# Kernel tuning notes

Measured on AMD Instinct MI355X. Metric: run time of the kernel, lower is better.

Reference implementation:

```python
import jax, jax.numpy as jnp
import numpy as np

N_NODES = 100000
N_EDGES = 1600000
IN_FEATS = 16
H_FEAT = 64
N_HEADS = 3
N_LAYERS = 8
NUM_CLASSES = 6
HID = H_FEAT * N_HEADS  # 192
NEG_SLOPE = 0.01  # torch F.leaky_relu default


def setup_inputs() -> dict:
    key = jax.random.key(0)
    ks = jax.random.split(key, 10)
    node_feat = jax.random.normal(ks[0], (N_NODES, IN_FEATS), dtype=jnp.float32)
    src = jax.random.randint(ks[1], (N_EDGES,), 0, N_NODES)
    dst = jax.random.randint(ks[2], (N_EDGES,), 0, N_NODES)
    # layer 1 params: per-head fc [H, out, in], attn [H, 2*out]
    W1 = jax.random.normal(ks[3], (N_HEADS, H_FEAT, IN_FEATS), dtype=jnp.float32) * 0.1
    a1 = jax.random.normal(ks[4], (N_HEADS, 2 * H_FEAT), dtype=jnp.float32) * 0.1
    # layers 2..8 params stacked: [L-1, H, out, hid]
    W = jax.random.normal(ks[5], (N_LAYERS - 1, N_HEADS, H_FEAT, HID), dtype=jnp.float32) * 0.1
    a = jax.random.normal(ks[6], (N_LAYERS - 1, N_HEADS, 2 * H_FEAT), dtype=jnp.float32) * 0.1
    fcW = jax.random.normal(ks[7], (NUM_CLASSES, HID), dtype=jnp.float32) * 0.1
    fcb = jnp.zeros((NUM_CLASSES,), dtype=jnp.float32)
    return {"node_feat": node_feat, "src": src, "dst": dst,
            "W1": W1, "a1": a1, "W": W, "a": a, "fcW": fcW, "fcb": fcb}


def _gat_layer(h, src, dst, Wl, al, n_nodes):
    """Multi-head GAT layer (merge='cat'). Wl:[H,O,I], al:[H,2O]."""
    O = Wl.shape[1]
    z = jnp.einsum('ni,hoi->nho', h, Wl)            # [N,H,O]
    a_src, a_dst = al[:, :O], al[:, O:]
    # attn_fc(cat(z_src, z_dst)) decomposed into per-node src/dst scores
    es = jnp.einsum('nho,ho->nh', z, a_src)          # [N,H]
    ed = jnp.einsum('nho,ho->nh', z, a_dst)          # [N,H]
    e = jax.nn.leaky_relu(es[src] + ed[dst], NEG_SLOPE)  # [E,H]
    # segment softmax over incoming edges of each dst node
    m = jax.ops.segment_max(e, dst, num_segments=n_nodes)
    m = jnp.where(jnp.isfinite(m), m, 0.0)
    ex = jnp.exp(e - m[dst])
    den = jax.ops.segment_sum(ex, dst, num_segments=n_nodes)
    alpha = ex / jnp.maximum(den[dst], 1e-9)          # [E,H]
    # scatter-sum aggregation of alpha-weighted source features
    hn = jax.ops.segment_sum(alpha[:, :, None] * z[src], dst, num_segments=n_nodes)  # [N,H,O]
    return hn.reshape(n_nodes, -1)                    # cat heads -> [N,H*O]


def reference(node_feat, src, dst, W1, a1, W, a, fcW, fcb):
    n = node_feat.shape[0]
    h = _gat_layer(node_feat, src, dst, W1, a1, n)
    h = jax.nn.elu(h)
    for l in range(W.shape[0]):
        h = _gat_layer(h, src, dst, W[l], a[l], n)
        h = jax.nn.elu(h)
    return h @ fcW.T + fcb
```

## Files before the change

### kernel.cpp

```cpp
#include <hip/hip_runtime.h>
#include <hip/hip_bf16.h>
#include <hip/hip_fp16.h>
#include <math.h>

#define NN 100000
#define NE 1600000
#define INF_ 16
#define HF 64
#define NH 3
#define HID 192
#define NC 6
#define NEG_SLOPE 0.01f

typedef _Float16 half8 __attribute__((ext_vector_type(8)));
typedef float f32x4 __attribute__((ext_vector_type(4)));


__global__ __launch_bounds__(256) void k_hist(const int* __restrict__ dst, int* __restrict__ deg) {
    int e = blockIdx.x * 256 + threadIdx.x;
    if (e < NE) atomicAdd(&deg[dst[e]], 1);
}

__global__ __launch_bounds__(256) void k_scan1(const int* __restrict__ deg, int* __restrict__ bsum) {
    __shared__ int sc[256];
    int t = threadIdx.x;
    int n = blockIdx.x * 256 + t;
    int v = (n < NN) ? deg[n] : 0;
    sc[t] = v; __syncthreads();
    for (int off = 1; off < 256; off <<= 1) {
        int x = (t >= off) ? sc[t - off] : 0;
        __syncthreads();
        sc[t] += x;
        __syncthreads();
    }
    if (t == 255) bsum[blockIdx.x] = sc[255];
}

__global__ __launch_bounds__(512) void k_scan2(const int* __restrict__ bsum, int* __restrict__ boff, int nb) {
    __shared__ int sc[512];
    int t = threadIdx.x;
    int v = (t < nb) ? bsum[t] : 0;
    sc[t] = v; __syncthreads();
    for (int off = 1; off < 512; off <<= 1) {
        int x = (t >= off) ? sc[t - off] : 0;
        __syncthreads();
        sc[t] += x;
        __syncthreads();
    }
    if (t < nb) boff[t] = sc[t] - v;
}

__global__ __launch_bounds__(256) void k_scan3(const int* __restrict__ deg, const int* __restrict__ boff,
                                               int* __restrict__ row_ptr, int* __restrict__ cursor) {
    __shared__ int sc[256];
    int t = threadIdx.x;
    int n = blockIdx.x * 256 + t;
    int v = (n < NN) ? deg[n] : 0;
    sc[t] = v; __syncthreads();
    for (int off = 1; off < 256; off <<= 1) {
        int x = (t >= off) ? sc[t - off] : 0;
        __syncthreads();
        sc[t] += x;
        __syncthreads();
    }
    if (n < NN) {
        int ex = boff[blockIdx.x] + sc[t] - v;
        row_ptr[n] = ex;
        cursor[n] = ex;
        if (n == NN - 1) row_ptr[NN] = ex + v;
    }
}

__global__ __launch_bounds__(256) void k_scatter(const int* __restrict__ src, const int* __restrict__ dst,
                                                 int* __restrict__ cursor, int* __restrict__ colb) {
    int e = blockIdx.x * 256 + threadIdx.x;
    if (e < NE) {
        int d = dst[e];
        int pos = atomicAdd(&cursor[d], 1);
        colb[pos] = src[e] * 384;
    }
}


__global__ __launch_bounds__(256) void k_cvtW(const float* __restrict__ W, __half* __restrict__ Wh, int n) {
    int i = blockIdx.x * 256 + threadIdx.x;
    if (i < n) Wh[i] = __float2half(W[i]);
}


__global__ __launch_bounds__(256) void k_prep(const float* __restrict__ W1, const float* __restrict__ a1,
                                              const float* __restrict__ W, const float* __restrict__ a,
                                              float* __restrict__ v0, __half* __restrict__ vh) {
    int bid = blockIdx.x, tid = threadIdx.x;
    if (bid == 0) {
        if (tid < 96) {
            int j = tid >> 4, k = tid & 15;
            int h = j % 3, sd = j / 3;
            float s = 0.f;
            for (int c = 0; c < 64; ++c)
                s += W1[h * 1024 + c * 16 + k] * a1[h * 128 + sd * 64 + c];
            v0[j * 16 + k] = s;
        }
    } else {
        int l = bid - 1;
        if (tid < HID) {
            int k = tid;
            __half* vt = vh + (size_t)l * 16 * HID;
            for (int j = 0; j < 6; ++j) {
                int h = j % 3, sd = j / 3;
                const float* wp = W + (size_t)l * 36864 + h * 12288 + k;
                const float* ap = a + (size_t)l * 384 + h * 128 + sd * 64;
                float s = 0.f;
                for (int c = 0; c < 64; ++c) s += wp[c * 192] * ap[c];
                __half hi = __float2half(s);
                __half lo = __float2half(s - __half2float(hi));
                vt[j * HID + k] = hi;
                vt[(j + 6) * HID + k] = lo;
            }
            for (int j = 12; j < 16; ++j) vt[j * HID + k] = __float2half(0.f);
        }
    }
}


__global__ __launch_bounds__(256) void k_transform1(const float* __restrict__ feat, const float* __restrict__ W1,
                                                    __half* __restrict__ zh) {
    int idx = blockIdx.x * 256 + threadIdx.x;
    if (idx >= NN * HID) return;
    int n = idx / HID;
    int c = idx - n * HID;
    const float* fr = feat + n * INF_;
    const float* wr = W1 + c * INF_;
    float s = 0.f;
#pragma unroll
    for (int i = 0; i < INF_; i += 4) {
        float4 f = *(const float4*)&fr[i];
        float4 w = *(const float4*)&wr[i];
        s += f.x * w.x + f.y * w.y + f.z * w.z + f.w * w.w;
    }
    zh[idx] = __float2half(s);
}


__global__ __launch_bounds__(256) void k_esed1(const float* __restrict__ feat, const float* __restrict__ v0,
                                               float* __restrict__ es, float* __restrict__ ed) {
    __shared__ float sv[96];
    int tid = threadIdx.x;
    if (tid < 96) sv[tid] = v0[tid];
    __syncthreads();
    int n = blockIdx.x * 256 + tid;
    if (n >= NN) return;
    float f[16];
#pragma unroll
    for (int i = 0; i < 16; i += 4) {
        float4 t4 = *(const float4*)&feat[n * 16 + i];
        f[i] = t4.x; f[i + 1] = t4.y; f[i + 2] = t4.z; f[i + 3] = t4.w;
    }
#pragma unroll
    for (int j = 0; j < 6; ++j) {
        float s = 0.f;
#pragma unroll
        for (int k = 0; k < 16; ++k) s += f[k] * sv[j * 16 + k];
        if (j < 3) es[n * 3 + j] = s;
        else ed[n * 3 + (j - 3)] = s;
    }
}


__global__ __launch_bounds__(256) void k_mfma(const __half* __restrict__ Ah, const __half* __restrict__ Whl,
                                              const __half* __restrict__ vhl,
                                              __half* __restrict__ zh, float* __restrict__ es,
                                              float* __restrict__ ed) {
    __shared__ char Bs[73728];
    int tid = threadIdx.x;

#pragma unroll
    for (int i = 0; i < 18; ++i) {
        int idx = tid + i * 256;
        int row = idx / 24;
        int pos = idx - row * 24;
        uint4 v = *(const uint4*)((const char*)Whl + (size_t)idx * 16);
        *(uint4*)(Bs + row * 384 + ((pos * 16) ^ ((row & 7) << 4))) = v;
    }
    __syncthreads();

    int wid = tid >> 6;
    int lane = tid & 63;
    int lrow = lane & 15;
    int lk = lane >> 4;
    int r0 = blockIdx.x * 128 + wid * 32;

    int arow0 = min(r0 + lrow, NN - 1);
    int arow1 = min(r0 + 16 + lrow, NN - 1);
    const __half* ap0 = &Ah[(size_t)arow0 * HID];
    const __half* ap1 = &Ah[(size_t)arow1 * HID];

    f32x4 acc[2][12];
    f32x4 acc13[2];
#pragma unroll
    for (int f = 0; f < 2; ++f) {
        acc13[f] = (f32x4){0.f, 0.f, 0.f, 0.f};
#pragma unroll
        for (int t = 0; t < 12; ++t) acc[f][t] = (f32x4){0.f, 0.f, 0.f, 0.f};
    }

#pragma unroll
    for (int ks = 0; ks < 6; ++ks) {
        half8 a0 = *(const half8*)&ap0[ks * 32 + lk * 8];
        half8 a1 = *(const half8*)&ap1[ks * 32 + lk * 8];
        half8 b13 = *(const half8*)&vhl[lrow * HID + ks * 32 + lk * 8];
        acc13[0] = __builtin_amdgcn_mfma_f32_16x16x32_f16(a0, b13, acc13[0], 0, 0, 0);
        acc13[1] = __builtin_amdgcn_mfma_f32_16x16x32_f16(a1, b13, acc13[1], 0, 0, 0);
#pragma unroll
        for (int t = 0; t < 12; ++t) {
            int brow = t * 16 + lrow;
            half8 bf = *(const half8*)(Bs + brow * 384 + ((ks * 64 + lk * 16) ^ ((brow & 7) << 4)));
            acc[0][t] = __builtin_amdgcn_mfma_f32_16x16x32_f16(a0, bf, acc[0][t], 0, 0, 0);
            acc[1][t] = __builtin_amdgcn_mfma_f32_16x16x32_f16(a1, bf, acc[1][t], 0, 0, 0);
        }
    }

#pragma unroll
    for (int f = 0; f < 2; ++f) {
        int orow0 = r0 + f * 16 + lk * 4;
#pragma unroll
        for (int t = 0; t < 12; ++t) {
#pragma unroll
            for (int g = 0; g < 4; ++g) {
                int row = orow0 + g;
                if (row < NN) zh[(size_t)row * HID + t * 16 + lrow] = __float2half(acc[f][t][g]);
            }
        }
#pragma unroll
        for (int g = 0; g < 4; ++g) {
            float vhi = acc13[f][g];
            float vlo = __shfl(vhi, lane + 6);
            float tot = vhi + vlo;
            int row = orow0 + g;
            if (row < NN) {
                if (lrow < 3) es[row * NH + lrow] = tot;
                else if (lrow < 6) ed[row * NH + (lrow - 3)] = tot;
            }
        }
    }
}


__global__ __launch_bounds__(256) void k_agg(const __half* __restrict__ zh, const int* __restrict__ colb,
                                             const float* __restrict__ es, const float* __restrict__ ed,
                                             const int* __restrict__ row_ptr, __half* __restrict__ h_out) {
    int w = blockIdx.x * 4 + (threadIdx.x >> 6);
    int slot = (threadIdx.x >> 3) & 7;
    int q = threadIdx.x & 7;
    int n = w * 8 + slot;
    int beg = row_ptr[n];
    int deg = row_ptr[n + 1] - beg;

    float3 d3 = *(const float3*)((const char*)ed + n * 12);

    float l0 = 0.f, l1 = 0.f, l2 = 0.f;
    float a0[8], a1[8], a2[8];
#pragma unroll
    for (int k = 0; k < 8; ++k) { a0[k] = 0.f; a1[k] = 0.f; a2[k] = 0.f; }

    const int* cp = colb + beg;
    const char* zb = (const char*)zh + q * 16;

    int so_n = 0;
    float3 s3_n = make_float3(0.f, 0.f, 0.f);
    if (deg > 0) {
        so_n = cp[0];
        s3_n = *(const float3*)((const char*)es + (so_n >> 5));
    }
    for (int i = 0; i < deg; ++i) {
        int so = so_n;
        float3 s3 = s3_n;
        if (i + 1 < deg) {
            so_n = cp[i + 1];
            s3_n = *(const float3*)((const char*)es + (so_n >> 5));
        }
        float x0 = s3.x + d3.x, x1 = s3.y + d3.y, x2 = s3.z + d3.z;
        x0 = fmaxf(x0, NEG_SLOPE * x0);
        x1 = fmaxf(x1, NEG_SLOPE * x1);
        x2 = fmaxf(x2, NEG_SLOPE * x2);
        float p0 = __expf(x0), p1 = __expf(x1), p2 = __expf(x2);
        const char* zp = zb + so;
        half8 z0 = *(const half8*)(zp);
        half8 z1 = *(const half8*)(zp + 128);
        half8 z2 = *(const half8*)(zp + 256);
        l0 += p0; l1 += p1; l2 += p2;
#pragma unroll
        for (int k = 0; k < 8; ++k) {
            a0[k] += p0 * (float)z0[k];
            a1[k] += p1 * (float)z1[k];
            a2[k] += p2 * (float)z2[k];
        }
    }

    float r0 = 1.f / fmaxf(l0, 1e-9f);
    float r1 = 1.f / fmaxf(l1, 1e-9f);
    float r2 = 1.f / fmaxf(l2, 1e-9f);
    char* ob = (char*)h_out + (size_t)n * 384 + q * 16;
    union { float4 f4; __half2 h2[4]; } u;
#pragma unroll
    for (int k = 0; k < 4; ++k) {
        float x0 = a0[2 * k] * r0, x1 = a0[2 * k + 1] * r0;
        x0 = (x0 > 0.f) ? x0 : (__expf(x0) - 1.f);
        x1 = (x1 > 0.f) ? x1 : (__expf(x1) - 1.f);
        u.h2[k] = __floats2half2_rn(x0, x1);
    }
    *(float4*)ob = u.f4;
#pragma unroll
    for (int k = 0; k < 4; ++k) {
        float x0 = a1[2 * k] * r1, x1 = a1[2 * k + 1] * r1;
        x0 = (x0 > 0.f) ? x0 : (__expf(x0) - 1.f);
        x1 = (x1 > 0.f) ? x1 : (__expf(x1) - 1.f);
        u.h2[k] = __floats2half2_rn(x0, x1);
    }
    *(float4*)(ob + 128) = u.f4;
#pragma unroll
    for (int k = 0; k < 4; ++k) {
        float x0 = a2[2 * k] * r2, x1 = a2[2 * k + 1] * r2;
        x0 = (x0 > 0.f) ? x0 : (__expf(x0) - 1.f);
        x1 = (x1 > 0.f) ? x1 : (__expf(x1) - 1.f);
        u.h2[k] = __floats2half2_rn(x0, x1);
    }
    *(float4*)(ob + 256) = u.f4;
}


__device__ inline float wred_sum(float v) {
#pragma unroll
    for (int o = 32; o; o >>= 1) v += __shfl_xor(v, o);
    return v;
}

__global__ __launch_bounds__(256) void k_fc(const __half* __restrict__ hbuf, const float* __restrict__ fcW,
                                            const float* __restrict__ fcb, float* __restrict__ out) {
    __shared__ float sW[NC * HID];
    __shared__ float sb[NC];
    int tid = threadIdx.x;
    for (int i = tid; i < NC * HID; i += 256) sW[i] = fcW[i];
    if (tid < NC) sb[tid] = fcb[tid];
    __syncthreads();
    int w = tid >> 6;
    int lane = tid & 63;
    int n = blockIdx.x * 4 + w;
    if (n >= NN) return;
    float h0 = __half2float(hbuf[(size_t)n * HID + lane]);
    float h1 = __half2float(hbuf[(size_t)n * HID + 64 + lane]);
    float h2 = __half2float(hbuf[(size_t)n * HID + 128 + lane]);
#pragma unroll
    for (int j = 0; j < NC; ++j) {
        float p = h0 * sW[j * HID + lane] + h1 * sW[j * HID + 64 + lane] + h2 * sW[j * HID + 128 + lane];
        p = wred_sum(p);
        if (lane == 0) out[n * NC + j] = p + sb[j];
    }
}


extern "C" void kernel_launch(void* const* d_in, const int* in_sizes, int n_in,
                              void* d_out, int out_size, void* d_ws, size_t ws_size,
                              hipStream_t stream) {
    const float* node_feat = (const float*)d_in[0];
    const int* src = (const int*)d_in[1];
    const int* dst = (const int*)d_in[2];
    const float* W1 = (const float*)d_in[3];
    const float* a1 = (const float*)d_in[4];
    const float* W = (const float*)d_in[5];
    const float* a = (const float*)d_in[6];
    const float* fcW = (const float*)d_in[7];
    const float* fcb = (const float*)d_in[8];
    float* out = (float*)d_out;

    char* p = (char*)d_ws;
    auto alloc = [&](size_t bytes) {
        void* r = (void*)p;
        p += (bytes + 255) & ~(size_t)255;
        return r;
    };
    int* deg = (int*)alloc(NN * 4);
    int* cursor = (int*)alloc(NN * 4);
    int* row_ptr = (int*)alloc((NN + 1) * 4);
    int* bsum = (int*)alloc(512 * 4);
    int* boff = (int*)alloc(512 * 4);
    int* colb = (int*)alloc((size_t)NE * 4);
    float* es = (float*)alloc((size_t)NN * NH * 4);
    float* ed = (float*)alloc((size_t)NN * NH * 4);
    __half* zh = (__half*)alloc((size_t)NN * HID * 2);
    __half* hb = (__half*)alloc((size_t)NN * HID * 2);
    const int NWH = 7 * NH * HF * HID;
    __half* Wh = (__half*)alloc((size_t)NWH * 2);
    float* v0 = (float*)alloc(96 * 4);
    __half* vh = (__half*)alloc((size_t)7 * 16 * HID * 2);

    int nb = (NN + 255) / 256;

    hipMemsetAsync(deg, 0, NN * 4, stream);
    k_hist<<<(NE + 255) / 256, 256, 0, stream>>>(dst, deg);
    k_scan1<<<nb, 256, 0, stream>>>(deg, bsum);
    k_scan2<<<1, 512, 0, stream>>>(bsum, boff, nb);
    k_scan3<<<nb, 256, 0, stream>>>(deg, boff, row_ptr, cursor);
    k_scatter<<<(NE + 255) / 256, 256, 0, stream>>>(src, dst, cursor, colb);
    k_cvtW<<<(NWH + 255) / 256, 256, 0, stream>>>(W, Wh, NWH);
    k_prep<<<8, 256, 0, stream>>>(W1, a1, W, a, v0, vh);

    int gAgg = NN / 8 / 4;

    k_transform1<<<(NN * HID + 255) / 256, 256, 0, stream>>>(node_feat, W1, zh);
    k_esed1<<<nb, 256, 0, stream>>>(node_feat, v0, es, ed);
    k_agg<<<gAgg, 256, 0, stream>>>(zh, colb, es, ed, row_ptr, hb);

    for (int l = 0; l < 7; ++l) {
        k_mfma<<<(NN + 127) / 128, 256, 0, stream>>>(hb, Wh + (size_t)l * NH * HF * HID,
                                                     vh + (size_t)l * 16 * HID, zh, es, ed);
        k_agg<<<gAgg, 256, 0, stream>>>(zh, colb, es, ed, row_ptr, hb);
    }

    k_fc<<<(NN + 3) / 4, 256, 0, stream>>>(hb, fcW, fcb, out);
}
```

Baseline: 1.395 ms.

## Build CSR via two-pass bucketed scatter and unroll aggregation by two edges

Replaces the per-edge global atomic scatter into CSR with a two-pass scheme. Edges are first binned by destination into 512-node buckets using shared-memory counters and staged as packed (local dst, src) words. A per-bucket kernel then places them using shared-memory cursors, which localizes the atomics and the writes. Separately, the aggregation loop processes two edges per iteration so more gathers are in flight, at the cost of more registers and an extra staging buffer.

Result: faster. 1.307 ms (-6.3%).

```diff
diff --git a/kernel.cpp b/kernel.cpp
--- a/kernel.cpp
+++ b/kernel.cpp
@@ -12,6 +12,10 @@
 #define NC 6
 #define NEG_SLOPE 0.01f
 
+#define BSH 9
+#define NBUCK 196
+#define TILE 2048
+
 typedef _Float16 half8 __attribute__((ext_vector_type(8)));
 typedef float f32x4 __attribute__((ext_vector_type(4)));
 
@@ -51,7 +55,7 @@
 }
 
 __global__ __launch_bounds__(256) void k_scan3(const int* __restrict__ deg, const int* __restrict__ boff,
-                                               int* __restrict__ row_ptr, int* __restrict__ cursor) {
+                                               int* __restrict__ row_ptr) {
     __shared__ int sc[256];
     int t = threadIdx.x;
     int n = blockIdx.x * 256 + t;
@@ -66,18 +70,67 @@
     if (n < NN) {
         int ex = boff[blockIdx.x] + sc[t] - v;
         row_ptr[n] = ex;
-        cursor[n] = ex;
         if (n == NN - 1) row_ptr[NN] = ex + v;
     }
 }
 
-__global__ __launch_bounds__(256) void k_scatter(const int* __restrict__ src, const int* __restrict__ dst,
-                                                 int* __restrict__ cursor, int* __restrict__ colb) {
-    int e = blockIdx.x * 256 + threadIdx.x;
-    if (e < NE) {
-        int d = dst[e];
-        int pos = atomicAdd(&cursor[d], 1);
-        colb[pos] = src[e] * 384;
+__global__ __launch_bounds__(256) void k_binit(const int* __restrict__ row_ptr, int* __restrict__ gcur) {
+    int b = threadIdx.x;
+    if (b < NBUCK) gcur[b] = row_ptr[min(b << BSH, NN)];
+}
+
+__global__ __launch_bounds__(256) void k_bucket(const int* __restrict__ src, const int* __restrict__ dst,
+                                                int* __restrict__ gcur, int* __restrict__ staged) {
+    __shared__ int cnt[NBUCK], base[NBUCK], cnt2[NBUCK];
+    int tid = threadIdx.x;
+    int e0 = blockIdx.x * TILE;
+    int cntE = min(TILE, NE - e0);
+    for (int i = tid; i < NBUCK; i += 256) { cnt[i] = 0; cnt2[i] = 0; }
+    __syncthreads();
+    int myDst[8], mySrc[8];
+#pragma unroll
+    for (int k = 0; k < 8; ++k) {
+        int idx = tid + k * 256;
+        if (idx < cntE) {
+            myDst[k] = dst[e0 + idx];
+            mySrc[k] = src[e0 + idx];
+            atomicAdd(&cnt[myDst[k] >> BSH], 1);
+        }
+    }
+    __syncthreads();
+    for (int i = tid; i < NBUCK; i += 256) {
+        if (cnt[i] > 0) base[i] = atomicAdd(&gcur[i], cnt[i]);
+    }
+    __syncthreads();
+#pragma unroll
+    for (int k = 0; k < 8; ++k) {
+        int idx = tid + k * 256;
+        if (idx < cntE) {
+            int b = myDst[k] >> BSH;
+            int r = atomicAdd(&cnt2[b], 1);
+            staged[base[b] + r] = ((myDst[k] & 511) << 17) | mySrc[k];
+        }
+    }
+}
+
+__global__ __launch_bounds__(256) void k_bscatter(const int* __restrict__ row_ptr, const int* __restrict__ staged,
+                                                  int* __restrict__ colb) {
+    __shared__ int cur[512];
+    int b = blockIdx.x;
+    int n0 = b << BSH;
+    int tid = threadIdx.x;
+    for (int i = tid; i < 512; i += 256) {
+        int n = n0 + i;
+        cur[i] = (n < NN) ? row_ptr[n] : 0;
+    }
+    __syncthreads();
+    int beg = row_ptr[n0];
+    int end = row_ptr[min(n0 + 512, NN)];
+    for (int i = beg + tid; i < end; i += 256) {
+        int v = staged[i];
+        int d = v >> 17;
+        int pos = atomicAdd(&cur[d], 1);
+        colb[pos] = (v & 0x1FFFF) * 384;
     }
 }
 
@@ -266,34 +319,51 @@
     const int* cp = colb + beg;
     const char* zb = (const char*)zh + q * 16;
 
-    int so_n = 0;
-    float3 s3_n = make_float3(0.f, 0.f, 0.f);
-    if (deg > 0) {
-        so_n = cp[0];
-        s3_n = *(const float3*)((const char*)es + (so_n >> 5));
-    }
-    for (int i = 0; i < deg; ++i) {
-        int so = so_n;
-        float3 s3 = s3_n;
-        if (i + 1 < deg) {
-            so_n = cp[i + 1];
-            s3_n = *(const float3*)((const char*)es + (so_n >> 5));
-        }
-        float x0 = s3.x + d3.x, x1 = s3.y + d3.y, x2 = s3.z + d3.z;
-        x0 = fmaxf(x0, NEG_SLOPE * x0);
-        x1 = fmaxf(x1, NEG_SLOPE * x1);
-        x2 = fmaxf(x2, NEG_SLOPE * x2);
-        float p0 = __expf(x0), p1 = __expf(x1), p2 = __expf(x2);
-        const char* zp = zb + so;
-        half8 z0 = *(const half8*)(zp);
-        half8 z1 = *(const half8*)(zp + 128);
-        half8 z2 = *(const half8*)(zp + 256);
-        l0 += p0; l1 += p1; l2 += p2;
+    int soA = 0, soB = 0;
+    float3 sA = make_float3(0.f, 0.f, 0.f), sB = sA;
+    if (deg > 0) { soA = cp[0]; sA = *(const float3*)((const char*)es + (soA >> 5)); }
+    if (deg > 1) { soB = cp[1]; sB = *(const float3*)((const char*)es + (soB >> 5)); }
+
+    int i = 0;
+    for (; i + 2 <= deg; i += 2) {
+        const char* zpA = zb + soA;
+        const char* zpB = zb + soB;
+        half8 zA0 = *(const half8*)(zpA);
+        half8 zA1 = *(const half8*)(zpA + 128);
+        half8 zA2 = *(const half8*)(zpA + 256);
+        half8 zB0 = *(const half8*)(zpB);
+        half8 zB1 = *(const half8*)(zpB + 128);
+        half8 zB2 = *(const half8*)(zpB + 256);
+        float xA0 = sA.x + d3.x, xA1 = sA.y + d3.y, xA2 = sA.z + d3.z;
+        float xB0 = sB.x + d3.x, xB1 = sB.y + d3.y, xB2 = sB.z + d3.z;
+        xA0 = fmaxf(xA0, NEG_SLOPE * xA0); xA1 = fmaxf(xA1, NEG_SLOPE * xA1); xA2 = fmaxf(xA2, NEG_SLOPE * xA2);
+        xB0 = fmaxf(xB0, NEG_SLOPE * xB0); xB1 = fmaxf(xB1, NEG_SLOPE * xB1); xB2 = fmaxf(xB2, NEG_SLOPE * xB2);
+        float pA0 = __expf(xA0), pA1 = __expf(xA1), pA2 = __expf(xA2);
+        float pB0 = __expf(xB0), pB1 = __expf(xB1), pB2 = __expf(xB2);
+        if (i + 2 < deg) { soA = cp[i + 2]; sA = *(const float3*)((const char*)es + (soA >> 5)); }
+        if (i + 3 < deg) { soB = cp[i + 3]; sB = *(const float3*)((const char*)es + (soB >> 5)); }
+        l0 += pA0 + pB0; l1 += pA1 + pB1; l2 += pA2 + pB2;
 #pragma unroll
         for (int k = 0; k < 8; ++k) {
-            a0[k] += p0 * (float)z0[k];
-            a1[k] += p1 * (float)z1[k];
-            a2[k] += p2 * (float)z2[k];
+            a0[k] += pA0 * (float)zA0[k] + pB0 * (float)zB0[k];
+            a1[k] += pA1 * (float)zA1[k] + pB1 * (float)zB1[k];
+            a2[k] += pA2 * (float)zA2[k] + pB2 * (float)zB2[k];
+        }
+    }
+    if (i < deg) {
+        const char* zpA = zb + soA;
+        half8 zA0 = *(const half8*)(zpA);
+        half8 zA1 = *(const half8*)(zpA + 128);
+        half8 zA2 = *(const half8*)(zpA + 256);
+        float xA0 = sA.x + d3.x, xA1 = sA.y + d3.y, xA2 = sA.z + d3.z;
+        xA0 = fmaxf(xA0, NEG_SLOPE * xA0); xA1 = fmaxf(xA1, NEG_SLOPE * xA1); xA2 = fmaxf(xA2, NEG_SLOPE * xA2);
+        float pA0 = __expf(xA0), pA1 = __expf(xA1), pA2 = __expf(xA2);
+        l0 += pA0; l1 += pA1; l2 += pA2;
+#pragma unroll
+        for (int k = 0; k < 8; ++k) {
+            a0[k] += pA0 * (float)zA0[k];
+            a1[k] += pA1 * (float)zA1[k];
+            a2[k] += pA2 * (float)zA2[k];
         }
     }
 
@@ -380,10 +450,11 @@
         return r;
     };
     int* deg = (int*)alloc(NN * 4);
-    int* cursor = (int*)alloc(NN * 4);
     int* row_ptr = (int*)alloc((NN + 1) * 4);
     int* bsum = (int*)alloc(512 * 4);
     int* boff = (int*)alloc(512 * 4);
+    int* gcur = (int*)alloc(NBUCK * 4);
+    int* staged = (int*)alloc((size_t)NE * 4);
     int* colb = (int*)alloc((size_t)NE * 4);
     float* es = (float*)alloc((size_t)NN * NH * 4);
     float* ed = (float*)alloc((size_t)NN * NH * 4);
@@ -400,8 +471,10 @@
     k_hist<<<(NE + 255) / 256, 256, 0, stream>>>(dst, deg);
     k_scan1<<<nb, 256, 0, stream>>>(deg, bsum);
     k_scan2<<<1, 512, 0, stream>>>(bsum, boff, nb);
-    k_scan3<<<nb, 256, 0, stream>>>(deg, boff, row_ptr, cursor);
-    k_scatter<<<(NE + 255) / 256, 256, 0, stream>>>(src, dst, cursor, colb);
+    k_scan3<<<nb, 256, 0, stream>>>(deg, boff, row_ptr);
+    k_binit<<<1, 256, 0, stream>>>(row_ptr, gcur);
+    k_bucket<<<(NE + TILE - 1) / TILE, 256, 0, stream>>>(src, dst, gcur, staged);
+    k_bscatter<<<NBUCK, 256, 0, stream>>>(row_ptr, staged, colb);
     k_cvtW<<<(NWH + 255) / 256, 256, 0, stream>>>(W, Wh, NWH);
     k_prep<<<8, 256, 0, stream>>>(W1, a1, W, a, v0, vh);
 
```
